# Optimization experiments

Measured on AMD Instinct MI355X. Metric: run time of the kernel, lower is better.

Reference implementation:

```python
import jax, jax.numpy as jnp
import numpy as np
import math

N_HEAD = 8
N_FEAT = 512
D_K = N_FEAT // N_HEAD
B, T = 4, 2048


def setup_inputs() -> dict:
    key = jax.random.key(0)
    ks = jax.random.split(key, 16)
    s = 1.0 / math.sqrt(N_FEAT)
    return {
        "x": jax.random.normal(ks[0], (B, T, N_FEAT), dtype=jnp.float32),
        "pos_emb": jax.random.normal(ks[1], (1, T, N_FEAT), dtype=jnp.float32),
        "Wq": jax.random.normal(ks[2], (N_FEAT, N_FEAT), dtype=jnp.float32) * s,
        "bq": jnp.zeros((N_FEAT,), dtype=jnp.float32),
        "Wk": jax.random.normal(ks[3], (N_FEAT, N_FEAT), dtype=jnp.float32) * s,
        "bk": jnp.zeros((N_FEAT,), dtype=jnp.float32),
        "Wv": jax.random.normal(ks[4], (N_FEAT, N_FEAT), dtype=jnp.float32) * s,
        "bv": jnp.zeros((N_FEAT,), dtype=jnp.float32),
        "Wpos": jax.random.normal(ks[5], (N_FEAT, N_FEAT), dtype=jnp.float32) * s,
        "Wout": jax.random.normal(ks[6], (N_FEAT, N_FEAT), dtype=jnp.float32) * s,
        "bout": jnp.zeros((N_FEAT,), dtype=jnp.float32),
        "pos_bias_u": jax.random.normal(ks[7], (N_HEAD, D_K), dtype=jnp.float32) * 0.05,
        "pos_bias_v": jax.random.normal(ks[8], (N_HEAD, D_K), dtype=jnp.float32) * 0.05,
    }


def reference(x, pos_emb, Wq, bq, Wk, bk, Wv, bv, Wpos, Wout, bout,
              pos_bias_u, pos_bias_v):
    b, t, f = x.shape
    h, d = N_HEAD, D_K
    # QKV projections (torch Linear: y = x @ W.T + b), split into heads -> (B,H,T,d)
    q = (jnp.einsum('btf,of->bto', x, Wq) + bq).reshape(b, t, h, d).transpose(0, 2, 1, 3)
    k = (jnp.einsum('btf,of->bto', x, Wk) + bk).reshape(b, t, h, d).transpose(0, 2, 1, 3)
    v = (jnp.einsum('btf,of->bto', x, Wv) + bv).reshape(b, t, h, d).transpose(0, 2, 1, 3)
    # positional projection: (1, T_pos, F) -> (H, T_pos, d)
    tp = pos_emb.shape[1]
    p = jnp.einsum('ptf,of->pto', pos_emb, Wpos).reshape(tp, h, d).transpose(1, 0, 2)
    q_u = q + pos_bias_u[None, :, None, :]  # (B,H,T,d)
    q_v = q + pos_bias_v[None, :, None, :]
    matrix_ac = jnp.einsum('bhtd,bhsd->bhts', q_u, k)   # content-content
    matrix_bd = jnp.einsum('bhtd,hsd->bhts', q_v, p)    # content-position
    scores = (matrix_ac + matrix_bd) / math.sqrt(d)
    attn = jax.nn.softmax(scores, axis=-1)  # dropout is identity in eval mode
    out = jnp.einsum('bhts,bhsd->bhtd', attn, v)
    out = out.transpose(0, 2, 1, 3).reshape(b, t, h * d)
    return jnp.einsum('btf,of->bto', out, Wout) + bout
```

## Files before the change

### kernel.cpp

```cpp
#include <hip/hip_runtime.h>

typedef float f4 __attribute__((ext_vector_type(4)));
typedef __attribute__((ext_vector_type(8))) short bf16x8;
typedef __attribute__((ext_vector_type(4))) float f32x4;
typedef __attribute__((ext_vector_type(2))) int i32x2;
typedef __attribute__((ext_vector_type(4))) int i32x4;

#define T_SEQ 2048
#define NFEAT 512
#define NHEAD 8
#define DK    64
#define BATCH 4

using gptr_t = const __attribute__((address_space(1))) void*;
using lptr_t = __attribute__((address_space(3))) void*;

#define LOG2E_8 0.18033688011f


static __device__ __forceinline__ short f2bf(float f) {
    unsigned u = __builtin_bit_cast(unsigned, f);
    u += 0x7fff + ((u >> 16) & 1);
    return (short)(u >> 16);
}
static __device__ __forceinline__ float b2f(short s) {
    unsigned u = ((unsigned)(unsigned short)s) << 16;
    return __builtin_bit_cast(float, u);
}
static __device__ __forceinline__ int pkbf(float a, float b) {
    unsigned ua = __builtin_bit_cast(unsigned, a) + 0x8000u;
    unsigned ub = __builtin_bit_cast(unsigned, b) + 0x8000u;
    return (int)((ua >> 16) | (ub & 0xFFFF0000u));
}
static __device__ __forceinline__ int pkbf_rne(float a, float b) {
    unsigned ua = __builtin_bit_cast(unsigned, a); ua += 0x7fff + ((ua >> 16) & 1);
    unsigned ub = __builtin_bit_cast(unsigned, b); ub += 0x7fff + ((ub >> 16) & 1);
    return (int)((ua >> 16) | (ub & 0xFFFF0000u));
}

__global__ __launch_bounds__(256) void cvt_kernel(
    const float* __restrict__ x, const float* __restrict__ pos,
    const float* __restrict__ Wq, const float* __restrict__ Wk, const float* __restrict__ Wv,
    const float* __restrict__ Wpos, const float* __restrict__ Wout,
    const float* __restrict__ bq, const float* __restrict__ bk, const float* __restrict__ bv,
    short* __restrict__ xb, short* __restrict__ posb, short* __restrict__ wqkv,
    short* __restrict__ wpb, short* __restrict__ wob, float* __restrict__ bqkv)
{
    const int blk = blockIdx.x;
    const float* src; short* dst; int off;
    if      (blk < 2048) { src = x;    dst = xb;          off = blk * 2048; }
    else if (blk < 2560) { src = pos;  dst = posb;        off = (blk - 2048) * 2048; }
    else if (blk < 2688) { src = Wq;   dst = wqkv;        off = (blk - 2560) * 2048; }
    else if (blk < 2816) { src = Wk;   dst = wqkv + 262144; off = (blk - 2688) * 2048; }
    else if (blk < 2944) { src = Wv;   dst = wqkv + 524288; off = (blk - 2816) * 2048; }
    else if (blk < 3072) { src = Wpos; dst = wpb;         off = (blk - 2944) * 2048; }
    else if (blk < 3200) { src = Wout; dst = wob;         off = (blk - 3072) * 2048; }
    else {
        int t = threadIdx.x;
        bqkv[t]        = bq[t];        bqkv[256 + t]  = bq[256 + t];
        bqkv[512 + t]  = bk[t];        bqkv[768 + t]  = bk[256 + t];
        bqkv[1024 + t] = bv[t];        bqkv[1280 + t] = bv[256 + t];
        return;
    }
    int i = off + threadIdx.x * 8;
    f4 a = *(const f4*)(src + i);
    f4 b = *(const f4*)(src + i + 4);
    bf16x8 o;
#pragma unroll
    for (int j = 0; j < 4; ++j) { o[j] = f2bf(a[j]); o[4 + j] = f2bf(b[j]); }
    *(bf16x8*)(dst + i) = o;
}

template<int OUT_BF16>
static __device__ __forceinline__ void gemm_tile(
    short* As, short* Bs,
    const short* __restrict__ A, const short* __restrict__ B,
    const float* __restrict__ bias, void* __restrict__ Cv,
    int N, int K, int row0, int col0)
{
    const int tid = threadIdx.x, lane = tid & 63, wave = tid >> 6;
    const int col = lane & 15, quad = lane >> 4;
    const int wm = (wave >> 1) * 64, wn = (wave & 1) * 64;
    const int rl = lane & 15;

    const short* Abase = A + (size_t)(row0 + wave * 32 + rl) * K + (lane >> 4) * 8;
    const short* Bbase = B + (size_t)(col0 + wave * 32 + rl) * K + (lane >> 4) * 8;

    f32x4 acc[4][4];
#pragma unroll
    for (int i = 0; i < 4; ++i)
#pragma unroll
        for (int j = 0; j < 4; ++j) acc[i][j] = (f32x4){0.f, 0.f, 0.f, 0.f};

    for (int k0 = 0; k0 < K; k0 += 64) {
        __syncthreads();
#pragma unroll
        for (int c = 0; c < 2; ++c)
#pragma unroll
            for (int hf = 0; hf < 2; ++hf) {
                __builtin_amdgcn_global_load_lds((gptr_t)(Abase + (size_t)(16 * c) * K + k0 + hf * 32),
                                                 (lptr_t)(As + wave * 2048 + c * 1024 + hf * 512), 16, 0, 0);
                __builtin_amdgcn_global_load_lds((gptr_t)(Bbase + (size_t)(16 * c) * K + k0 + hf * 32),
                                                 (lptr_t)(Bs + wave * 2048 + c * 1024 + hf * 512), 16, 0, 0);
            }
        __syncthreads();
#pragma unroll
        for (int kt = 0; kt < 2; ++kt) {
            bf16x8 af[4], bfr[4];
#pragma unroll
            for (int mt = 0; mt < 4; ++mt)
                af[mt] = *(const bf16x8*)&As[((wm >> 4) + mt) * 1024 + (kt * 4 + quad) * 128 + col * 8];
#pragma unroll
            for (int nt = 0; nt < 4; ++nt)
                bfr[nt] = *(const bf16x8*)&Bs[((wn >> 4) + nt) * 1024 + (kt * 4 + quad) * 128 + col * 8];
#pragma unroll
            for (int mt = 0; mt < 4; ++mt)
#pragma unroll
                for (int nt = 0; nt < 4; ++nt)
                    acc[mt][nt] = __builtin_amdgcn_mfma_f32_16x16x32_bf16(af[mt], bfr[nt], acc[mt][nt], 0, 0, 0);
        }
    }

    float bv4[4];
#pragma unroll
    for (int nt = 0; nt < 4; ++nt)
        bv4[nt] = bias ? bias[col0 + wn + nt * 16 + col] : 0.f;
#pragma unroll
    for (int mt = 0; mt < 4; ++mt)
#pragma unroll
        for (int reg = 0; reg < 4; ++reg) {
            int r = row0 + wm + mt * 16 + quad * 4 + reg;
#pragma unroll
            for (int nt = 0; nt < 4; ++nt) {
                int c = col0 + wn + nt * 16 + col;
                float v = acc[mt][nt][reg] + bv4[nt];
                if (OUT_BF16) ((short*)Cv)[(size_t)r * N + c] = f2bf(v);
                else          ((float*)Cv)[(size_t)r * N + c] = v;
            }
        }
}

__global__ __launch_bounds__(256) void gemm_qkv_pos(
    const short* __restrict__ xb, const short* __restrict__ wqkv,
    const float* __restrict__ bqkv, short* __restrict__ QKV,
    const short* __restrict__ posb, const short* __restrict__ wpb,
    short* __restrict__ Pm)
{
    __shared__ short As[8192], Bs[8192];
    const int bid = blockIdx.x;
    if (bid < 768) {
        const int xcd = bid & 7, s = bid >> 3;
        const int row = xcd * 8 + (s & 7), colt = s >> 3;
        gemm_tile<1>(As, Bs, xb, wqkv, bqkv, QKV, 1536, 512, row * 128, colt * 128);
    } else {
        const int t = bid - 768;
        gemm_tile<1>(As, Bs, posb, wpb, nullptr, Pm, 512, 512, (t / 4) * 128, (t % 4) * 128);
    }
}

__global__ __launch_bounds__(256) void gemm_out_kernel(
    const short* __restrict__ Op, const float* __restrict__ Lb,
    const short* __restrict__ B, const float* __restrict__ bias,
    float* __restrict__ C)
{
    __shared__ short As[8192], Bs[8192];
    const int bid = blockIdx.x;
    const int xcd = bid & 7, s = bid >> 3;
    const int row0 = (xcd * 8 + (s & 7)) * 128, col0 = (s >> 3) * 128;
    const int N = 512, K = 512;

    const int tid = threadIdx.x, lane = tid & 63, wave = tid >> 6;
    const int col = lane & 15, quad = lane >> 4;
    const int wm = (wave >> 1) * 64, wn = (wave & 1) * 64;
    const int rl = lane & 15;

    const short* Bbase = B + (size_t)(col0 + wave * 32 + rl) * K + quad * 8;
    const int rA0 = row0 + wave * 32 + rl;

    f32x4 acc[4][4];
#pragma unroll
    for (int i = 0; i < 4; ++i)
#pragma unroll
        for (int j = 0; j < 4; ++j) acc[i][j] = (f32x4){0.f, 0.f, 0.f, 0.f};

    for (int k0 = 0; k0 < K; k0 += 64) {
        const int h = k0 >> 6;
        __syncthreads();
#pragma unroll
        for (int c = 0; c < 2; ++c)
#pragma unroll
            for (int hf = 0; hf < 2; ++hf)
                __builtin_amdgcn_global_load_lds((gptr_t)(Bbase + (size_t)(16 * c) * K + k0 + hf * 32),
                                                 (lptr_t)(Bs + wave * 2048 + c * 1024 + hf * 512), 16, 0, 0);
#pragma unroll
        for (int c = 0; c < 2; ++c) {
            const int r  = rA0 + c * 16;
            const int t  = r & 2047;
            const int bh = (r >> 11) * 8 + h;
            const float l = Lb[bh * T_SEQ + t] + Lb[65536 + bh * T_SEQ + t];
            const float inv = 1.f / l;
#pragma unroll
            for (int hf = 0; hf < 2; ++hf) {
                const short* src = Op + (size_t)r * NFEAT + k0 + hf * 32 + quad * 8;
                bf16x8 o1 = *(const bf16x8*)src;
                bf16x8 o2 = *(const bf16x8*)(src + 4194304);
                bf16x8 oc;
#pragma unroll
                for (int j = 0; j < 8; ++j) oc[j] = f2bf((b2f(o1[j]) + b2f(o2[j])) * inv);
                *(bf16x8*)&As[wave * 2048 + c * 1024 + hf * 512 + lane * 8] = oc;
            }
        }
        __syncthreads();
#pragma unroll
        for (int kt = 0; kt < 2; ++kt) {
            bf16x8 af[4], bfr[4];
#pragma unroll
            for (int mt = 0; mt < 4; ++mt)
                af[mt] = *(const bf16x8*)&As[((wm >> 4) + mt) * 1024 + (kt * 4 + quad) * 128 + col * 8];
#pragma unroll
            for (int nt = 0; nt < 4; ++nt)
                bfr[nt] = *(const bf16x8*)&Bs[((wn >> 4) + nt) * 1024 + (kt * 4 + quad) * 128 + col * 8];
#pragma unroll
            for (int mt = 0; mt < 4; ++mt)
#pragma unroll
                for (int nt = 0; nt < 4; ++nt)
                    acc[mt][nt] = __builtin_amdgcn_mfma_f32_16x16x32_bf16(af[mt], bfr[nt], acc[mt][nt], 0, 0, 0);
        }
    }

    float bv4[4];
#pragma unroll
    for (int nt = 0; nt < 4; ++nt)
        bv4[nt] = bias[col0 + wn + nt * 16 + col];
#pragma unroll
    for (int mt = 0; mt < 4; ++mt)
#pragma unroll
        for (int reg = 0; reg < 4; ++reg) {
            int r = row0 + wm + mt * 16 + quad * 4 + reg;
#pragma unroll
            for (int nt = 0; nt < 4; ++nt) {
                int c = col0 + wn + nt * 16 + col;
                C[(size_t)r * N + c] = acc[mt][nt][reg] + bv4[nt];
            }
        }
}

__global__ __launch_bounds__(256) void kvprep_kernel(
    const short* __restrict__ qkv, const short* __restrict__ pm,
    const float* __restrict__ u, const float* __restrict__ vb,
    short* __restrict__ kp, short* __restrict__ vt, float* __restrict__ cb)
{
    __shared__ short tile[64][72];
    const int tid = threadIdx.x, lr = tid >> 2, lc = (tid & 3) * 16;
    const int bh = blockIdx.y, b = bh >> 3, h = bh & 7, s0 = blockIdx.x * 64;

    const short* kptr = qkv + (size_t)(b * T_SEQ + s0 + lr) * 1536 + 512 + h * DK + lc;
    const short* pptr = pm + (size_t)(s0 + lr) * NFEAT + h * DK + lc;
    const short* vptr = qkv + (size_t)(b * T_SEQ + s0 + lr) * 1536 + 1024 + h * DK + lc;
    bf16x8 k0_ = *(const bf16x8*)kptr,       k1_ = *(const bf16x8*)(kptr + 8);
    bf16x8 p0_ = *(const bf16x8*)pptr,       p1_ = *(const bf16x8*)(pptr + 8);
    bf16x8 v0_ = *(const bf16x8*)vptr,       v1_ = *(const bf16x8*)(vptr + 8);

    float c = 0.f;
    bf16x8 o0, o1;
#pragma unroll
    for (int j = 0; j < 8; ++j) {
        float kf = b2f(k0_[j]), pf = b2f(p0_[j]);
        o0[j] = f2bf(kf + pf);
        c += u[h * DK + lc + j] * kf + vb[h * DK + lc + j] * pf;
        float kf1 = b2f(k1_[j]), pf1 = b2f(p1_[j]);
        o1[j] = f2bf(kf1 + pf1);
        c += u[h * DK + lc + 8 + j] * kf1 + vb[h * DK + lc + 8 + j] * pf1;
    }
    short* kpd = kp + ((size_t)bh * T_SEQ + s0 + lr) * DK + lc;
    *(bf16x8*)kpd       = o0;
    *(bf16x8*)(kpd + 8) = o1;
    c += __shfl_xor(c, 1);
    c += __shfl_xor(c, 2);
    if ((tid & 3) == 0) cb[(size_t)bh * T_SEQ + s0 + lr] = LOG2E_8 * c;

    *(bf16x8*)&tile[lr][lc]     = v0_;
    *(bf16x8*)&tile[lr][lc + 8] = v1_;
    __syncthreads();
    short* dst = vt + (size_t)(bh * DK + lr) * T_SEQ + s0 + lc;
    bf16x8 t0_, t1_;
#pragma unroll
    for (int j = 0; j < 8; ++j) { t0_[j] = tile[lc + j][lr]; t1_[j] = tile[lc + 8 + j][lr]; }
    *(bf16x8*)dst       = t0_;
    *(bf16x8*)(dst + 8) = t1_;
}

__global__ __launch_bounds__(256, 4) void attn_kernel(
    const short* __restrict__ qkv, const short* __restrict__ kp,
    const short* __restrict__ vt, const float* __restrict__ cb,
    short* __restrict__ Op, float* __restrict__ Lb)
{
    __shared__ __align__(16) short KPs[64][72], Vts[64][72];
    __shared__ float cs[64];
    const int tid = threadIdx.x, lane = tid & 63, wave = tid >> 6;
    const int col = lane & 15, quad = lane >> 4;
    const int idx = blockIdx.x;
    const int xcd = idx & 7, slot = idx >> 3;
    const int half = slot & 1;
    const int t0 = ((slot >> 1) & 15) * 128;
    const int bh = (slot >> 5) * 8 + xcd;
    const int base = half * 1024;
    const int b = bh >> 3, h = bh & 7;

    bf16x8 qa[2][2];
#pragma unroll
    for (int g = 0; g < 2; ++g) {
        const short* qb = qkv + (size_t)(b * T_SEQ + t0 + wave * 32 + g * 16 + col) * 1536 + h * DK + quad * 8;
        qa[g][0] = *(const bf16x8*)qb;
        qa[g][1] = *(const bf16x8*)(qb + 32);
    }

    bf16x8 onesb;
#pragma unroll
    for (int j = 0; j < 8; ++j) onesb[j] = (short)0x3F80;

    const int lr  = tid >> 2;
    const int lcq = (tid & 3) * 16;
    const int kap  = (lr & 32) | ((lr & 12) << 1) | ((lr & 16) >> 2) | (lr & 3);
    const int kapt = (tid & 32) | ((tid & 12) << 1) | ((tid & 16) >> 2) | (tid & 3);

    const short* kpbase = kp + (size_t)bh * T_SEQ * DK;
    const short* vtbase = vt + (size_t)bh * DK * T_SEQ;

    const short* kpp = kpbase + (size_t)(base + kap) * DK + lcq;
    const short* vtp = vtbase + (size_t)lr * T_SEQ + base + lcq;
    const float* cbp = cb + (size_t)bh * T_SEQ + base + kapt;

    bf16x8 kpr0 = *(const bf16x8*)kpp;
    bf16x8 kpr1 = *(const bf16x8*)(kpp + 8);
    bf16x8 vtr0 = *(const bf16x8*)vtp;
    bf16x8 vtr1 = *(const bf16x8*)(vtp + 8);
    float cbr = (tid < 64) ? *cbp : 0.f;

    f32x4 Oacc[2][4];
    f32x4 Lacc[2];
#pragma unroll
    for (int g = 0; g < 2; ++g) {
        Lacc[g] = (f32x4){0.f, 0.f, 0.f, 0.f};
#pragma unroll
        for (int i = 0; i < 4; ++i) Oacc[g][i] = (f32x4){0.f, 0.f, 0.f, 0.f};
    }

    for (int it = 0; it < 16; ++it) {
        __syncthreads();
        *(bf16x8*)&KPs[lr][lcq]     = kpr0;
        *(bf16x8*)&KPs[lr][lcq + 8] = kpr1;
        *(bf16x8*)&Vts[lr][lcq]     = vtr0;
        *(bf16x8*)&Vts[lr][lcq + 8] = vtr1;
        if (tid < 64) cs[tid] = cbr;
        __syncthreads();

        kpp += 64 * DK; vtp += 64; cbp += 64;
        kpr0 = *(const bf16x8*)kpp;
        kpr1 = *(const bf16x8*)(kpp + 8);
        vtr0 = *(const bf16x8*)vtp;
        vtr1 = *(const bf16x8*)(vtp + 8);
        if (tid < 64) cbr = *cbp;

        f32x4 S[2][4];
#pragma unroll
        for (int g = 0; g < 2; ++g)
#pragma unroll
            for (int nt = 0; nt < 4; ++nt) S[g][nt] = (f32x4){0.f, 0.f, 0.f, 0.f};
#pragma unroll
        for (int nt = 0; nt < 4; ++nt) {
            bf16x8 a0 = *(const bf16x8*)&KPs[nt * 16 + col][quad * 8];
            bf16x8 a1 = *(const bf16x8*)&KPs[nt * 16 + col][32 + quad * 8];
            S[0][nt] = __builtin_amdgcn_mfma_f32_16x16x32_bf16(a0, qa[0][0], S[0][nt], 0, 0, 0);
            S[1][nt] = __builtin_amdgcn_mfma_f32_16x16x32_bf16(a0, qa[1][0], S[1][nt], 0, 0, 0);
            S[0][nt] = __builtin_amdgcn_mfma_f32_16x16x32_bf16(a1, qa[0][1], S[0][nt], 0, 0, 0);
            S[1][nt] = __builtin_amdgcn_mfma_f32_16x16x32_bf16(a1, qa[1][1], S[1][nt], 0, 0, 0);
        }
        int pk_[2][4][2];
#pragma unroll
        for (int nt = 0; nt < 4; ++nt) {
            const f4 cvn = *(const f4*)&cs[nt * 16 + quad * 4];
#pragma unroll
            for (int g = 0; g < 2; ++g) {
                float e0 = __builtin_amdgcn_exp2f(fmaf(S[g][nt][0], LOG2E_8, cvn[0]));
                float e1 = __builtin_amdgcn_exp2f(fmaf(S[g][nt][1], LOG2E_8, cvn[1]));
                float e2 = __builtin_amdgcn_exp2f(fmaf(S[g][nt][2], LOG2E_8, cvn[2]));
                float e3 = __builtin_amdgcn_exp2f(fmaf(S[g][nt][3], LOG2E_8, cvn[3]));
                pk_[g][nt][0] = pkbf(e0, e1);
                pk_[g][nt][1] = pkbf(e2, e3);
            }
        }
#pragma unroll
        for (int kt = 0; kt < 2; ++kt) {
            i32x4 w0 = (i32x4){pk_[0][2 * kt][0], pk_[0][2 * kt][1], pk_[0][2 * kt + 1][0], pk_[0][2 * kt + 1][1]};
            i32x4 w1 = (i32x4){pk_[1][2 * kt][0], pk_[1][2 * kt][1], pk_[1][2 * kt + 1][0], pk_[1][2 * kt + 1][1]};
            bf16x8 pf0 = __builtin_bit_cast(bf16x8, w0);
            bf16x8 pf1 = __builtin_bit_cast(bf16x8, w1);
            Lacc[0] = __builtin_amdgcn_mfma_f32_16x16x32_bf16(onesb, pf0, Lacc[0], 0, 0, 0);
            Lacc[1] = __builtin_amdgcn_mfma_f32_16x16x32_bf16(onesb, pf1, Lacc[1], 0, 0, 0);
#pragma unroll
            for (int dt = 0; dt < 4; ++dt) {
                bf16x8 vb = *(const bf16x8*)&Vts[dt * 16 + col][kt * 32 + quad * 8];
                Oacc[0][dt] = __builtin_amdgcn_mfma_f32_16x16x32_bf16(vb, pf0, Oacc[0][dt], 0, 0, 0);
                Oacc[1][dt] = __builtin_amdgcn_mfma_f32_16x16x32_bf16(vb, pf1, Oacc[1][dt], 0, 0, 0);
            }
        }
    }
    short* ophalf = Op + (size_t)half * 4194304;
    float* lhalf  = Lb + (size_t)half * 65536 + (size_t)bh * T_SEQ;
#pragma unroll
    for (int g = 0; g < 2; ++g) {
        const int t = t0 + wave * 32 + g * 16 + col;
        if (quad == 0) lhalf[t] = Lacc[g][0];
        short* op = ophalf + (size_t)(b * T_SEQ + t) * NFEAT + h * DK;
#pragma unroll
        for (int dt = 0; dt < 4; ++dt) {
            i32x2 w;
            w[0] = pkbf_rne(Oacc[g][dt][0], Oacc[g][dt][1]);
            w[1] = pkbf_rne(Oacc[g][dt][2], Oacc[g][dt][3]);
            *(i32x2*)(op + dt * 16 + quad * 4) = w;
        }
    }
}

extern "C" void kernel_launch(void* const* d_in, const int* in_sizes, int n_in,
                              void* d_out, int out_size, void* d_ws, size_t ws_size,
                              hipStream_t stream)
{
    const float* x    = (const float*)d_in[0];
    const float* pos  = (const float*)d_in[1];
    const float* Wq   = (const float*)d_in[2];
    const float* bq   = (const float*)d_in[3];
    const float* Wk   = (const float*)d_in[4];
    const float* bk   = (const float*)d_in[5];
    const float* Wv   = (const float*)d_in[6];
    const float* bv   = (const float*)d_in[7];
    const float* Wpos = (const float*)d_in[8];
    const float* Wout = (const float*)d_in[9];
    const float* bout = (const float*)d_in[10];
    const float* pbu  = (const float*)d_in[11];
    const float* pbv  = (const float*)d_in[12];
    float* out = (float*)d_out;

    short* xb   = (short*)d_ws;
    short* posb = xb   + 4194304;
    short* wqkv = posb + 1048576;
    short* wpb  = wqkv + 786432;
    short* wob  = wpb  + 262144;
    short* QKV  = wob  + 262144;
    short* Pm   = QKV  + 12582912;
    short* KP   = Pm   + 1048576;
    short* Vt   = KP   + 4194304;
    short* AttO = Vt   + 4194304;
    float* bqkv = (float*)(AttO + 4194304);
    float* Cb   = bqkv + 1536;
    short* Op   = (short*)(Cb + 65536);
    float* Lb   = (float*)(Op + 8388608);

    cvt_kernel<<<dim3(3201), dim3(256), 0, stream>>>(x, pos, Wq, Wk, Wv, Wpos, Wout, bq, bk, bv,
                                                     xb, posb, wqkv, wpb, wob, bqkv);
    gemm_qkv_pos<<<dim3(832), dim3(256), 0, stream>>>(xb, wqkv, bqkv, QKV, posb, wpb, Pm);
    kvprep_kernel<<<dim3(T_SEQ / 64, BATCH * NHEAD), dim3(256), 0, stream>>>(QKV, Pm, pbu, pbv, KP, Vt, Cb);
    attn_kernel<<<dim3(1024), dim3(256), 0, stream>>>(QKV, KP, Vt, Cb, Op, Lb);
    gemm_out_kernel<<<dim3(256), dim3(256), 0, stream>>>(Op, Lb, wob, bout, out);
}
```

Measured before the change: 217.0 us.

## Load K/P and V tiles directly from global memory, dropping LDS staging

Removes the shared-memory staging of the key/position, transposed-V and column-bias tiles, along with the two block barriers per iteration. Each wave now reads its MFMA operands straight from global memory (served by L1/L2) using permuted row offsets. This removes the LDS traffic and the syncs, but each wave re-fetches the same data independently. It also drops the register prefetch, so global load latency is exposed inside the loop.

```diff
diff --git a/kernel.cpp b/kernel.cpp
--- a/kernel.cpp
+++ b/kernel.cpp
@@ -295,8 +295,6 @@
     const short* __restrict__ vt, const float* __restrict__ cb,
     short* __restrict__ Op, float* __restrict__ Lb)
 {
-    __shared__ __align__(16) short KPs[64][72], Vts[64][72];
-    __shared__ float cs[64];
     const int tid = threadIdx.x, lane = tid & 63, wave = tid >> 6;
     const int col = lane & 15, quad = lane >> 4;
     const int idx = blockIdx.x;
@@ -319,23 +317,10 @@
 #pragma unroll
     for (int j = 0; j < 8; ++j) onesb[j] = (short)0x3F80;
 
-    const int lr  = tid >> 2;
-    const int lcq = (tid & 3) * 16;
-    const int kap  = (lr & 32) | ((lr & 12) << 1) | ((lr & 16) >> 2) | (lr & 3);
-    const int kapt = (tid & 32) | ((tid & 12) << 1) | ((tid & 16) >> 2) | (tid & 3);
-
-    const short* kpbase = kp + (size_t)bh * T_SEQ * DK;
-    const short* vtbase = vt + (size_t)bh * DK * T_SEQ;
-
-    const short* kpp = kpbase + (size_t)(base + kap) * DK + lcq;
-    const short* vtp = vtbase + (size_t)lr * T_SEQ + base + lcq;
-    const float* cbp = cb + (size_t)bh * T_SEQ + base + kapt;
-
-    bf16x8 kpr0 = *(const bf16x8*)kpp;
-    bf16x8 kpr1 = *(const bf16x8*)(kpp + 8);
-    bf16x8 vtr0 = *(const bf16x8*)vtp;
-    bf16x8 vtr1 = *(const bf16x8*)(vtp + 8);
-    float cbr = (tid < 64) ? *cbp : 0.f;
+    const int colpart = ((col & 12) << 1) | (col & 3);
+    const short* kpW = kp + (size_t)bh * T_SEQ * DK + (size_t)(base + colpart) * DK + quad * 8;
+    const float* cbW = cb + (size_t)bh * T_SEQ + base + quad * 8;
+    const short* vtW = vt + (size_t)bh * DK * T_SEQ + (size_t)col * T_SEQ + base + quad * 8;
 
     f32x4 Oacc[2][4];
     f32x4 Lacc[2];
@@ -347,20 +332,8 @@
     }
 
     for (int it = 0; it < 16; ++it) {
-        __syncthreads();
-        *(bf16x8*)&KPs[lr][lcq]     = kpr0;
-        *(bf16x8*)&KPs[lr][lcq + 8] = kpr1;
-        *(bf16x8*)&Vts[lr][lcq]     = vtr0;
-        *(bf16x8*)&Vts[lr][lcq + 8] = vtr1;
-        if (tid < 64) cs[tid] = cbr;
-        __syncthreads();
-
-        kpp += 64 * DK; vtp += 64; cbp += 64;
-        kpr0 = *(const bf16x8*)kpp;
-        kpr1 = *(const bf16x8*)(kpp + 8);
-        vtr0 = *(const bf16x8*)vtp;
-        vtr1 = *(const bf16x8*)(vtp + 8);
-        if (tid < 64) cbr = *cbp;
+        const int kq = it * 64 * DK;
+        const int tq = it * 64;
 
         f32x4 S[2][4];
 #pragma unroll
@@ -369,8 +342,9 @@
             for (int nt = 0; nt < 4; ++nt) S[g][nt] = (f32x4){0.f, 0.f, 0.f, 0.f};
 #pragma unroll
         for (int nt = 0; nt < 4; ++nt) {
-            bf16x8 a0 = *(const bf16x8*)&KPs[nt * 16 + col][quad * 8];
-            bf16x8 a1 = *(const bf16x8*)&KPs[nt * 16 + col][32 + quad * 8];
+            const int ntoff = ((nt & 2) << 4) | ((nt & 1) << 2);
+            bf16x8 a0 = *(const bf16x8*)(kpW + kq + ntoff * DK);
+            bf16x8 a1 = *(const bf16x8*)(kpW + kq + ntoff * DK + 32);
             S[0][nt] = __builtin_amdgcn_mfma_f32_16x16x32_bf16(a0, qa[0][0], S[0][nt], 0, 0, 0);
             S[1][nt] = __builtin_amdgcn_mfma_f32_16x16x32_bf16(a0, qa[1][0], S[1][nt], 0, 0, 0);
             S[0][nt] = __builtin_amdgcn_mfma_f32_16x16x32_bf16(a1, qa[0][1], S[0][nt], 0, 0, 0);
@@ -379,7 +353,8 @@
         int pk_[2][4][2];
 #pragma unroll
         for (int nt = 0; nt < 4; ++nt) {
-            const f4 cvn = *(const f4*)&cs[nt * 16 + quad * 4];
+            const int ntoff = ((nt & 2) << 4) | ((nt & 1) << 2);
+            const f4 cvn = *(const f4*)(cbW + tq + ntoff);
 #pragma unroll
             for (int g = 0; g < 2; ++g) {
                 float e0 = __builtin_amdgcn_exp2f(fmaf(S[g][nt][0], LOG2E_8, cvn[0]));
@@ -400,7 +375,7 @@
             Lacc[1] = __builtin_amdgcn_mfma_f32_16x16x32_bf16(onesb, pf1, Lacc[1], 0, 0, 0);
 #pragma unroll
             for (int dt = 0; dt < 4; ++dt) {
-                bf16x8 vb = *(const bf16x8*)&Vts[dt * 16 + col][kt * 32 + quad * 8];
+                bf16x8 vb = *(const bf16x8*)(vtW + tq + dt * 16 * T_SEQ + kt * 32);
                 Oacc[0][dt] = __builtin_amdgcn_mfma_f32_16x16x32_bf16(vb, pf0, Oacc[0][dt], 0, 0, 0);
                 Oacc[1][dt] = __builtin_amdgcn_mfma_f32_16x16x32_bf16(vb, pf1, Oacc[1][dt], 0, 0, 0);
             }
```

After: 291.1 us. +34.1%, slower.
